# Performance work log

Measured on AMD Instinct MI355X. Metric: run time of the kernel, lower is better.

## Reference

```python
import jax, jax.numpy as jnp
import numpy as np

C_CT, C_MRI, C_OUT = 64, 64, 64
B, D, H, W = 1, 8, 32, 32


def setup_inputs() -> dict:
    key = jax.random.key(0)
    ks = jax.random.split(key, 18)
    s = 0.05
    inp = {
        "ct_features": jax.random.normal(ks[0], (B, C_CT, D, H, W), jnp.float32),
        "mri_features": jax.random.normal(ks[1], (B, C_MRI, D, H, W), jnp.float32),
        # 1x1x1 Conv3d == per-voxel linear: weight (out, in), bias (out,)
        "wq_ct": jax.random.normal(ks[2], (C_OUT, C_CT), jnp.float32) * s,
        "bq_ct": jax.random.normal(ks[3], (C_OUT,), jnp.float32) * s,
        "wk_mri": jax.random.normal(ks[4], (C_OUT, C_MRI), jnp.float32) * s,
        "bk_mri": jax.random.normal(ks[5], (C_OUT,), jnp.float32) * s,
        "wv_mri": jax.random.normal(ks[6], (C_OUT, C_MRI), jnp.float32) * s,
        "bv_mri": jax.random.normal(ks[7], (C_OUT,), jnp.float32) * s,
        "wq_mri": jax.random.normal(ks[8], (C_OUT, C_MRI), jnp.float32) * s,
        "bq_mri": jax.random.normal(ks[9], (C_OUT,), jnp.float32) * s,
        "wk_ct": jax.random.normal(ks[10], (C_OUT, C_CT), jnp.float32) * s,
        "bk_ct": jax.random.normal(ks[11], (C_OUT,), jnp.float32) * s,
        "wv_ct": jax.random.normal(ks[12], (C_OUT, C_CT), jnp.float32) * s,
        "bv_ct": jax.random.normal(ks[13], (C_OUT,), jnp.float32) * s,
        "wo": jax.random.normal(ks[14], (C_OUT, 2 * C_OUT), jnp.float32) * s,
        "bo": jax.random.normal(ks[15], (C_OUT,), jnp.float32) * s,
    }
    return inp


def _proj(x_flat, w, b):
    # x_flat: (B, Cin, N); 1x1x1 conv -> (B, Cout, N)
    return jnp.einsum("oc,bcn->bon", w, x_flat) + b[None, :, None]


def _forward(ct, mri, wq_ct, bq_ct, wk_mri, bk_mri, wv_mri, bv_mri,
             wq_mri, bq_mri, wk_ct, bk_ct, wv_ct, bv_ct, wo, bo):
    b, _, d, h, w = ct.shape
    n = d * h * w
    ct_f = ct.reshape(b, ct.shape[1], n)
    mri_f = mri.reshape(b, mri.shape[1], n)
    scale = 1.0 / np.sqrt(C_OUT).astype(np.float32)

    # CT queries attend over MRI keys/values
    ct_q = _proj(ct_f, wq_ct, bq_ct)      # (B, C, N)
    mri_k = _proj(mri_f, wk_mri, bk_mri)  # (B, C, N)
    mri_v = _proj(mri_f, wv_mri, bv_mri)  # (B, C, N)
    attn_ct = jax.nn.softmax(jnp.einsum("bci,bcj->bij", ct_q, mri_k) * scale, axis=-1)
    ct_att = jnp.einsum("bcj,bij->bci", mri_v, attn_ct)  # (B, C, N)

    # MRI queries attend over CT keys/values
    mri_q = _proj(mri_f, wq_mri, bq_mri)
    ct_k = _proj(ct_f, wk_ct, bk_ct)
    ct_v = _proj(ct_f, wv_ct, bv_ct)
    attn_mri = jax.nn.softmax(jnp.einsum("bci,bcj->bij", mri_q, ct_k) * scale, axis=-1)
    mri_att = jnp.einsum("bcj,bij->bci", ct_v, attn_mri)

    fused = jnp.concatenate([ct_att, mri_att], axis=1)  # (B, 2C, N)
    out = _proj(fused, wo, bo)  # (B, C, N)
    return out.reshape(b, C_OUT, d, h, w)


def reference(ct_features, mri_features, wq_ct, bq_ct, wk_mri, bk_mri,
              wv_mri, bv_mri, wq_mri, bq_mri, wk_ct, bk_ct, wv_ct, bv_ct,
              wo, bo):
    return _forward(ct_features, mri_features, wq_ct, bq_ct, wk_mri, bk_mri,
                    wv_mri, bv_mri, wq_mri, bq_mri, wk_ct, bk_ct,
                    wv_ct, bv_ct, wo, bo)
```

## Files before the change

kernel.cpp:

```cpp
#include <hip/hip_runtime.h>
#include <stdint.h>

constexpr int N = 8192;
constexpr float QSCALE = 0.18033688011112042f;
constexpr int SPLIT = 4;

typedef __attribute__((ext_vector_type(4))) float f32x4;
typedef __attribute__((ext_vector_type(16))) float f32x16;
typedef __attribute__((ext_vector_type(4))) unsigned int u32x4;
typedef __attribute__((ext_vector_type(2))) unsigned int u32x2;
typedef __attribute__((ext_vector_type(4))) unsigned short u16x4;
typedef __attribute__((ext_vector_type(8))) __bf16 bf16x8;

__device__ inline unsigned short f2bf(float f) {
  unsigned u = __builtin_bit_cast(unsigned, f);
  u += 0x7FFFu + ((u >> 16) & 1u);
  return (unsigned short)(u >> 16);
}
__device__ inline float bf2f(unsigned short u) {
  return __builtin_bit_cast(float, (unsigned)u << 16);
}
__device__ inline unsigned cvtpk(float a, float b) {
  unsigned r;
  asm("v_cvt_pk_bf16_f32 %0, %1, %2" : "=v"(r) : "v"(a), "v"(b));
  return r;
}

__device__ inline void mfma32(f32x16& d, u32x4 a, u32x4 b) {
  d = __builtin_amdgcn_mfma_f32_32x32x16_bf16(
      __builtin_bit_cast(bf16x8, a), __builtin_bit_cast(bf16x8, b), d, 0, 0, 0);
}
__device__ inline void gload16(const void* src, void* lds) {
  __builtin_amdgcn_global_load_lds(
      (const __attribute__((address_space(1))) unsigned int*)src,
      (__attribute__((address_space(3))) unsigned int*)lds, 16, 0, 0);
}

struct ProjArgs {
  const float* x[6];
  const float* w[6];
  const float* b[6];
  unsigned short* o[6];
  int mode[6];
  float scale[6];
};

__global__ __launch_bounds__(256) void proj_kernel(ProjArgs A) {
  const int p = blockIdx.y;
  const float* __restrict__ x = A.x[p];
  const float* __restrict__ w = A.w[p];
  const float* __restrict__ bias = A.b[p];
  unsigned short* __restrict__ out = A.o[p];
  const int n0 = blockIdx.x * 64;
  __shared__ float Xs[64][64];
  __shared__ float Ws[64][64];
  const int t = threadIdx.x;
#pragma unroll
  for (int i = 0; i < 4; i++) {
    int s = t + i * 256;
    ((u32x4*)Ws)[s] = ((const u32x4*)w)[s];
  }
#pragma unroll
  for (int i = 0; i < 4; i++) {
    int s = t + i * 256;
    int c = s >> 4, nc = s & 15;
    *(u32x4*)&Xs[c][nc * 4] = *(const u32x4*)&x[c * N + n0 + nc * 4];
  }
  __syncthreads();
  const int n = t & 63, h = t >> 6;
  float acc[16];
#pragma unroll
  for (int o = 0; o < 16; o++) acc[o] = bias[h * 16 + o];
  for (int c = 0; c < 64; c++) {
    float xv = Xs[c][n];
#pragma unroll
    for (int o = 0; o < 16; o++) acc[o] = fmaf(Ws[h * 16 + o][c], xv, acc[o]);
  }
  const float sc = A.scale[p];
  if (A.mode[p] == 0) {
    unsigned short* po = out + (size_t)(n0 + n) * 64 + h * 16;
#pragma unroll
    for (int o = 0; o < 16; o++) po[o] = f2bf(acc[o] * sc);
  } else {
#pragma unroll
    for (int o = 0; o < 16; o++) out[(size_t)(h * 16 + o) * N + n0 + n] = f2bf(acc[o] * sc);
  }
}

__global__ __launch_bounds__(256, 2) void attn_kernel(
    const unsigned short* __restrict__ Q0, const unsigned short* __restrict__ K0,
    const unsigned short* __restrict__ V0, const unsigned short* __restrict__ Q1,
    const unsigned short* __restrict__ K1, const unsigned short* __restrict__ V1,
    unsigned short* __restrict__ Opart, float* __restrict__ Lsum) {
  const int bid = blockIdx.x;
  const int slice = bid & 7;
  const int qb = bid >> 3;
  const int dir = slice >> 2;
  const int chunk = slice & 3;
  const unsigned short* __restrict__ Q = dir ? Q1 : Q0;
  const unsigned short* __restrict__ K = dir ? K1 : K0;
  const unsigned short* __restrict__ V = dir ? V1 : V0;

  __shared__ char smem[33280];

  const int t = threadIdx.x;
  const int lane = t & 63, w = t >> 6;
  const int qsub = w >> 1, jsub = w & 1;
  const int hi = lane >> 5, l31 = lane & 31;
  const int kvbase = chunk * 2048;

  const int srowoff = lane >> 3;
  const int swzb = ((lane & 7) ^ (lane >> 3)) * 16;
  const char* const Kc = (const char*)K;
  const char* const Vc = (const char*)V;

#define STAGE(jtile, slot)                                                     \
  do {                                                                         \
    const int j0s = kvbase + (jtile) * 64;                                     \
    _Pragma("unroll") for (int i = 0; i < 2; i++) {                            \
      const int row = (w * 2 + i) * 8 + srowoff;                               \
      gload16(Kc + (size_t)(j0s + row) * 128 + swzb,                           \
              smem + (slot) * 8192 + (w * 2 + i) * 1024);                      \
      gload16(Vc + (size_t)row * (N * 2) + (size_t)j0s * 2 + swzb,             \
              smem + 16384 + (slot) * 8192 + (w * 2 + i) * 1024);              \
    }                                                                          \
  } while (0)

  u32x4 qf[2][4];
#pragma unroll
  for (int qs = 0; qs < 2; qs++) {
    const int qrow = qb * 128 + qsub * 64 + qs * 32 + l31;
#pragma unroll
    for (int ks = 0; ks < 4; ks++)
      qf[qs][ks] = *(const u32x4*)((const char*)Q + (size_t)qrow * 128 + (2 * ks + hi) * 16);
  }

  f32x16 acc[2][2];
#pragma unroll
  for (int cb = 0; cb < 2; cb++)
#pragma unroll
    for (int qs = 0; qs < 2; qs++)
#pragma unroll
      for (int r = 0; r < 16; r++) acc[cb][qs][r] = 0.f;
  float lpart[2] = {0.f, 0.f};

  STAGE(0, 0);
  for (int jt = 0; jt < 32; ++jt) {
    asm volatile("s_waitcnt vmcnt(0)" ::: "memory");
    __builtin_amdgcn_s_barrier();
    __builtin_amdgcn_sched_barrier(0);
    const int cur = jt & 1;
    if (jt + 1 < 32) STAGE(jt + 1, cur ^ 1);
    char* const Kl = smem + cur * 8192;
    char* const Vl = smem + 16384 + cur * 8192;

    u32x4 kf[4];
    {
      const int row = jsub * 32 + l31;
      const int rs = (row & 7) << 4;
#pragma unroll
      for (int ks = 0; ks < 4; ks++)
        kf[ks] = *(const u32x4*)(Kl + row * 128 + (((2 * ks + hi) * 16) ^ rs));
    }

    f32x16 st[2];
#pragma unroll
    for (int qs = 0; qs < 2; qs++)
#pragma unroll
      for (int r = 0; r < 16; r++) st[qs][r] = 0.f;
    __builtin_amdgcn_s_setprio(1);
#pragma unroll
    for (int ks = 0; ks < 4; ks++) {
      mfma32(st[0], kf[ks], qf[0][ks]);
      mfma32(st[1], kf[ks], qf[1][ks]);
    }
    __builtin_amdgcn_s_setprio(0);

    u32x4 vf[2][2];
#pragma unroll
    for (int cb = 0; cb < 2; cb++) {
      const int row = cb * 32 + l31;
      const int rs = (row & 7) << 4;
#pragma unroll
      for (int js = 0; js < 2; js++)
        vf[cb][js] = *(const u32x4*)(Vl + row * 128 + (((jsub * 4 + js * 2 + hi) * 16) ^ rs));
    }

#pragma unroll
    for (int qs = 0; qs < 2; qs++) {
      float p[16];
#pragma unroll
      for (int r = 0; r < 16; r++) p[r] = __builtin_amdgcn_exp2f(st[qs][r]);
      lpart[qs] += (((p[0] + p[1]) + (p[2] + p[3])) + ((p[4] + p[5]) + (p[6] + p[7]))) +
                   (((p[8] + p[9]) + (p[10] + p[11])) + ((p[12] + p[13]) + (p[14] + p[15])));
      unsigned w00 = cvtpk(p[0], p[1]),   w01 = cvtpk(p[2], p[3]);
      unsigned w10 = cvtpk(p[4], p[5]),   w11 = cvtpk(p[6], p[7]);
      unsigned w20 = cvtpk(p[8], p[9]),   w21 = cvtpk(p[10], p[11]);
      unsigned w30 = cvtpk(p[12], p[13]), w31 = cvtpk(p[14], p[15]);
      asm volatile("v_permlane32_swap_b32 %0, %1" : "+v"(w00), "+v"(w10));
      asm volatile("v_permlane32_swap_b32 %0, %1" : "+v"(w01), "+v"(w11));
      asm volatile("v_permlane32_swap_b32 %0, %1" : "+v"(w20), "+v"(w30));
      asm volatile("v_permlane32_swap_b32 %0, %1" : "+v"(w21), "+v"(w31));
      u32x4 pf0, pf1;
      pf0[0] = w00; pf0[1] = w01; pf0[2] = w10; pf0[3] = w11;
      pf1[0] = w20; pf1[1] = w21; pf1[2] = w30; pf1[3] = w31;
      __builtin_amdgcn_s_setprio(1);
      mfma32(acc[0][qs], vf[0][0], pf0);
      mfma32(acc[1][qs], vf[1][0], pf0);
      mfma32(acc[0][qs], vf[0][1], pf1);
      mfma32(acc[1][qs], vf[1][1], pf1);
      __builtin_amdgcn_s_setprio(0);
    }
  }
#undef STAGE

#pragma unroll
  for (int qs = 0; qs < 2; qs++) lpart[qs] += __shfl_xor(lpart[qs], 32);

  __syncthreads();
  char* const obuf = smem + qsub * 16384;
  float* const mlb = (float*)(smem + 32768);
  if (jsub == 1) {
#pragma unroll
    for (int qs = 0; qs < 2; qs++) {
      const int qloc = qs * 32 + l31;
      const int qsw = (qloc & 7) << 4;
#pragma unroll
      for (int cb = 0; cb < 2; cb++)
#pragma unroll
        for (int a = 0; a < 4; a++) {
          const int ch0 = cb * 32 + 8 * a + 4 * hi;
          f32x4 v;
          v[0] = acc[cb][qs][4 * a];     v[1] = acc[cb][qs][4 * a + 1];
          v[2] = acc[cb][qs][4 * a + 2]; v[3] = acc[cb][qs][4 * a + 3];
          *(f32x4*)(obuf + qloc * 256 + ((ch0 * 4) ^ qsw)) = v;
        }
      if (hi == 0) mlb[qsub * 64 + qloc] = lpart[qs];
    }
  }
  __syncthreads();
  if (jsub == 0) {
#pragma unroll
    for (int qs = 0; qs < 2; qs++) {
      const int qloc = qs * 32 + l31;
      const int qsw = (qloc & 7) << 4;
      const int qg = qb * 128 + qsub * 64 + qloc;
      const size_t pbase = ((size_t)slice * N + qg) * 64;
#pragma unroll
      for (int cb = 0; cb < 2; cb++)
#pragma unroll
        for (int a = 0; a < 4; a++) {
          const int ch0 = cb * 32 + 8 * a + 4 * hi;
          f32x4 oo = *(const f32x4*)(obuf + qloc * 256 + ((ch0 * 4) ^ qsw));
          u32x2 pk;
          pk[0] = cvtpk(acc[cb][qs][4 * a] + oo[0], acc[cb][qs][4 * a + 1] + oo[1]);
          pk[1] = cvtpk(acc[cb][qs][4 * a + 2] + oo[2], acc[cb][qs][4 * a + 3] + oo[3]);
          *(u32x2*)(Opart + pbase + ch0) = pk;
        }
      if (hi == 0) Lsum[(size_t)slice * N + qg] = lpart[qs] + mlb[qsub * 64 + qloc];
    }
  }
}

__global__ __launch_bounds__(256) void oproj_kernel(
    const unsigned short* __restrict__ Opart, const float* __restrict__ Lsum,
    const float* __restrict__ wo, const float* __restrict__ bo,
    float* __restrict__ out) {
  __shared__ float Fs[128][32];
  __shared__ float Ws[64][128];
  const int t = threadIdx.x;
  const int n0 = blockIdx.x * 32;
#pragma unroll
  for (int i = 0; i < 8; i++) {
    int s = t + i * 256;
    ((u32x4*)Ws)[s] = ((const u32x4*)wo)[s];
  }
  const int q = t & 31;
  const int cg = t >> 5;
#pragma unroll
  for (int dir = 0; dir < 2; dir++) {
    float lt = 0.f;
#pragma unroll
    for (int c = 0; c < 4; c++) lt += Lsum[(size_t)(dir * SPLIT + c) * N + n0 + q];
    const float rD = 1.0f / lt;
#pragma unroll
    for (int i = 0; i < 2; i++) {
      const int ch4 = cg * 2 + i;
      float s0 = 0.f, s1 = 0.f, s2 = 0.f, s3 = 0.f;
#pragma unroll
      for (int c = 0; c < 4; c++) {
        u16x4 v = *(const u16x4*)(Opart +
            ((size_t)(dir * SPLIT + c) * N + n0 + q) * 64 + ch4 * 4);
        s0 += bf2f(v[0]); s1 += bf2f(v[1]); s2 += bf2f(v[2]); s3 += bf2f(v[3]);
      }
      Fs[dir * 64 + ch4 * 4 + 0][q] = s0 * rD;
      Fs[dir * 64 + ch4 * 4 + 1][q] = s1 * rD;
      Fs[dir * 64 + ch4 * 4 + 2][q] = s2 * rD;
      Fs[dir * 64 + ch4 * 4 + 3][q] = s3 * rD;
    }
  }
  __syncthreads();
  const int n = t & 31, h = t >> 5;
  float acc[8];
#pragma unroll
  for (int o = 0; o < 8; o++) acc[o] = bo[h * 8 + o];
  for (int ch = 0; ch < 128; ch++) {
    float fv = Fs[ch][n];
#pragma unroll
    for (int o = 0; o < 8; o++) acc[o] = fmaf(Ws[h * 8 + o][ch], fv, acc[o]);
  }
#pragma unroll
  for (int o = 0; o < 8; o++) out[(size_t)(h * 8 + o) * N + n0 + n] = acc[o];
}

extern "C" void kernel_launch(void* const* d_in, const int* in_sizes, int n_in,
                              void* d_out, int out_size, void* d_ws, size_t ws_size,
                              hipStream_t stream) {
  const float* ct     = (const float*)d_in[0];
  const float* mri    = (const float*)d_in[1];
  const float* wq_ct  = (const float*)d_in[2];
  const float* bq_ct  = (const float*)d_in[3];
  const float* wk_mri = (const float*)d_in[4];
  const float* bk_mri = (const float*)d_in[5];
  const float* wv_mri = (const float*)d_in[6];
  const float* bv_mri = (const float*)d_in[7];
  const float* wq_mri = (const float*)d_in[8];
  const float* bq_mri = (const float*)d_in[9];
  const float* wk_ct  = (const float*)d_in[10];
  const float* bk_ct  = (const float*)d_in[11];
  const float* wv_ct  = (const float*)d_in[12];
  const float* bv_ct  = (const float*)d_in[13];
  const float* wo     = (const float*)d_in[14];
  const float* bo     = (const float*)d_in[15];

  char* ws = (char*)d_ws;
  const size_t MB = (size_t)1 << 20;
  unsigned short* Qt_ct  = (unsigned short*)(ws + 0 * MB);
  unsigned short* Kt_mri = (unsigned short*)(ws + 1 * MB);
  unsigned short* V_mri  = (unsigned short*)(ws + 2 * MB);
  unsigned short* Qt_mri = (unsigned short*)(ws + 3 * MB);
  unsigned short* Kt_ct  = (unsigned short*)(ws + 4 * MB);
  unsigned short* V_ct   = (unsigned short*)(ws + 5 * MB);
  unsigned short* Opart  = (unsigned short*)(ws + 6 * MB);
  float* Lsum            = (float*)(ws + 14 * MB);

  ProjArgs A;
  A.x[0] = ct;  A.w[0] = wq_ct;  A.b[0] = bq_ct;  A.o[0] = Qt_ct;  A.mode[0] = 0; A.scale[0] = QSCALE;
  A.x[1] = mri; A.w[1] = wk_mri; A.b[1] = bk_mri; A.o[1] = Kt_mri; A.mode[1] = 0; A.scale[1] = 1.f;
  A.x[2] = mri; A.w[2] = wv_mri; A.b[2] = bv_mri; A.o[2] = V_mri;  A.mode[2] = 1; A.scale[2] = 1.f;
  A.x[3] = mri; A.w[3] = wq_mri; A.b[3] = bq_mri; A.o[3] = Qt_mri; A.mode[3] = 0; A.scale[3] = QSCALE;
  A.x[4] = ct;  A.w[4] = wk_ct;  A.b[4] = bk_ct;  A.o[4] = Kt_ct;  A.mode[4] = 0; A.scale[4] = 1.f;
  A.x[5] = ct;  A.w[5] = wv_ct;  A.b[5] = bv_ct;  A.o[5] = V_ct;   A.mode[5] = 1; A.scale[5] = 1.f;

  proj_kernel<<<dim3(128, 6), 256, 0, stream>>>(A);
  attn_kernel<<<dim3(512), 256, 0, stream>>>(Qt_ct, Kt_mri, V_mri,
                                             Qt_mri, Kt_ct, V_ct, Opart, Lsum);
  oproj_kernel<<<dim3(256), 256, 0, stream>>>(Opart, Lsum, wo, bo, (float*)d_out);
}
```

Before: 68.73 us.

## Load K/V fragments directly from global memory into registers instead of LDS staging

Removes the double-buffered LDS staging of K and V tiles, along with its per-iteration waitcnt and barrier. Each wave now loads its K fragments (prefetched one tile ahead) and V fragments straight from global memory into registers. This eliminates block-wide synchronization and LDS traffic. In exchange, global loads become less coalesced: the V loads use row strides of N*2 bytes, the two waves sharing a jsub read the same K/V redundantly, and the V-load latency is exposed within each iteration.

```diff
diff --git a/kernel.cpp b/kernel.cpp
--- a/kernel.cpp
+++ b/kernel.cpp
@@ -29,11 +29,6 @@
 __device__ inline void mfma32(f32x16& d, u32x4 a, u32x4 b) {
   d = __builtin_amdgcn_mfma_f32_32x32x16_bf16(
       __builtin_bit_cast(bf16x8, a), __builtin_bit_cast(bf16x8, b), d, 0, 0, 0);
-}
-__device__ inline void gload16(const void* src, void* lds) {
-  __builtin_amdgcn_global_load_lds(
-      (const __attribute__((address_space(1))) unsigned int*)src,
-      (__attribute__((address_space(3))) unsigned int*)lds, 16, 0, 0);
 }
 
 struct ProjArgs {
@@ -108,21 +103,23 @@
   const int qsub = w >> 1, jsub = w & 1;
   const int hi = lane >> 5, l31 = lane & 31;
   const int kvbase = chunk * 2048;
-
-  const int srowoff = lane >> 3;
-  const int swzb = ((lane & 7) ^ (lane >> 3)) * 16;
   const char* const Kc = (const char*)K;
   const char* const Vc = (const char*)V;
 
-#define STAGE(jtile, slot)                                                     \
+#define LOADK(jt, kf)                                                          \
   do {                                                                         \
-    const int j0s = kvbase + (jtile) * 64;                                     \
-    _Pragma("unroll") for (int i = 0; i < 2; i++) {                            \
-      const int row = (w * 2 + i) * 8 + srowoff;                               \
-      gload16(Kc + (size_t)(j0s + row) * 128 + swzb,                           \
-              smem + (slot) * 8192 + (w * 2 + i) * 1024);                      \
-      gload16(Vc + (size_t)row * (N * 2) + (size_t)j0s * 2 + swzb,             \
-              smem + 16384 + (slot) * 8192 + (w * 2 + i) * 1024);              \
+    const size_t row_ = (size_t)(kvbase + (jt) * 64 + jsub * 32 + l31);        \
+    _Pragma("unroll") for (int ks = 0; ks < 4; ks++)                           \
+      kf[ks] = *(const u32x4*)(Kc + row_ * 128 + (2 * ks + hi) * 16);          \
+  } while (0)
+#define LOADV(jt, vf)                                                          \
+  do {                                                                         \
+    const int jb_ = kvbase + (jt) * 64 + jsub * 32;                            \
+    _Pragma("unroll") for (int cb = 0; cb < 2; cb++) {                         \
+      const size_t vr_ = (size_t)(cb * 32 + l31) * (N * 2);                    \
+      _Pragma("unroll") for (int js = 0; js < 2; js++)                         \
+        vf[cb][js] = *(const u32x4*)(Vc + vr_ +                                \
+                                     (size_t)(jb_ + (js * 2 + hi) * 8) * 2);   \
     }                                                                          \
   } while (0)
 
@@ -144,75 +141,55 @@
       for (int r = 0; r < 16; r++) acc[cb][qs][r] = 0.f;
   float lpart[2] = {0.f, 0.f};
 
-  STAGE(0, 0);
-  for (int jt = 0; jt < 32; ++jt) {
-    asm volatile("s_waitcnt vmcnt(0)" ::: "memory");
-    __builtin_amdgcn_s_barrier();
-    __builtin_amdgcn_sched_barrier(0);
-    const int cur = jt & 1;
-    if (jt + 1 < 32) STAGE(jt + 1, cur ^ 1);
-    char* const Kl = smem + cur * 8192;
-    char* const Vl = smem + 16384 + cur * 8192;
-
-    u32x4 kf[4];
-    {
-      const int row = jsub * 32 + l31;
-      const int rs = (row & 7) << 4;
-#pragma unroll
-      for (int ks = 0; ks < 4; ks++)
-        kf[ks] = *(const u32x4*)(Kl + row * 128 + (((2 * ks + hi) * 16) ^ rs));
-    }
-
-    f32x16 st[2];
-#pragma unroll
-    for (int qs = 0; qs < 2; qs++)
-#pragma unroll
-      for (int r = 0; r < 16; r++) st[qs][r] = 0.f;
-    __builtin_amdgcn_s_setprio(1);
-#pragma unroll
-    for (int ks = 0; ks < 4; ks++) {
-      mfma32(st[0], kf[ks], qf[0][ks]);
-      mfma32(st[1], kf[ks], qf[1][ks]);
-    }
-    __builtin_amdgcn_s_setprio(0);
-
-    u32x4 vf[2][2];
-#pragma unroll
-    for (int cb = 0; cb < 2; cb++) {
-      const int row = cb * 32 + l31;
-      const int rs = (row & 7) << 4;
-#pragma unroll
-      for (int js = 0; js < 2; js++)
-        vf[cb][js] = *(const u32x4*)(Vl + row * 128 + (((jsub * 4 + js * 2 + hi) * 16) ^ rs));
-    }
-
-#pragma unroll
-    for (int qs = 0; qs < 2; qs++) {
-      float p[16];
-#pragma unroll
-      for (int r = 0; r < 16; r++) p[r] = __builtin_amdgcn_exp2f(st[qs][r]);
-      lpart[qs] += (((p[0] + p[1]) + (p[2] + p[3])) + ((p[4] + p[5]) + (p[6] + p[7]))) +
-                   (((p[8] + p[9]) + (p[10] + p[11])) + ((p[12] + p[13]) + (p[14] + p[15])));
-      unsigned w00 = cvtpk(p[0], p[1]),   w01 = cvtpk(p[2], p[3]);
-      unsigned w10 = cvtpk(p[4], p[5]),   w11 = cvtpk(p[6], p[7]);
-      unsigned w20 = cvtpk(p[8], p[9]),   w21 = cvtpk(p[10], p[11]);
-      unsigned w30 = cvtpk(p[12], p[13]), w31 = cvtpk(p[14], p[15]);
-      asm volatile("v_permlane32_swap_b32 %0, %1" : "+v"(w00), "+v"(w10));
-      asm volatile("v_permlane32_swap_b32 %0, %1" : "+v"(w01), "+v"(w11));
-      asm volatile("v_permlane32_swap_b32 %0, %1" : "+v"(w20), "+v"(w30));
-      asm volatile("v_permlane32_swap_b32 %0, %1" : "+v"(w21), "+v"(w31));
-      u32x4 pf0, pf1;
-      pf0[0] = w00; pf0[1] = w01; pf0[2] = w10; pf0[3] = w11;
-      pf1[0] = w20; pf1[1] = w21; pf1[2] = w30; pf1[3] = w31;
-      __builtin_amdgcn_s_setprio(1);
-      mfma32(acc[0][qs], vf[0][0], pf0);
-      mfma32(acc[1][qs], vf[1][0], pf0);
-      mfma32(acc[0][qs], vf[0][1], pf1);
-      mfma32(acc[1][qs], vf[1][1], pf1);
-      __builtin_amdgcn_s_setprio(0);
-    }
-  }
-#undef STAGE
+#define BODY(jt, kfC, kfN)                                                     \
+  do {                                                                         \
+    u32x4 vf[2][2];                                                            \
+    LOADV(jt, vf);                                     \
+    if ((jt) + 1 < 32) LOADK((jt) + 1, kfN);           \
+    f32x16 st[2];                                                              \
+    _Pragma("unroll") for (int qs = 0; qs < 2; qs++)                           \
+      _Pragma("unroll") for (int r = 0; r < 16; r++) st[qs][r] = 0.f;          \
+    __builtin_amdgcn_s_setprio(1);                                             \
+    _Pragma("unroll") for (int ks = 0; ks < 4; ks++) {                         \
+      mfma32(st[0], kfC[ks], qf[0][ks]);                                       \
+      mfma32(st[1], kfC[ks], qf[1][ks]);                                       \
+    }                                                                          \
+    __builtin_amdgcn_s_setprio(0);                                             \
+    _Pragma("unroll") for (int qs = 0; qs < 2; qs++) {                         \
+      float p[16];                                                             \
+      _Pragma("unroll") for (int r = 0; r < 16; r++)                           \
+        p[r] = __builtin_amdgcn_exp2f(st[qs][r]);                              \
+      lpart[qs] += (((p[0]+p[1])+(p[2]+p[3]))+((p[4]+p[5])+(p[6]+p[7]))) +     \
+                   (((p[8]+p[9])+(p[10]+p[11]))+((p[12]+p[13])+(p[14]+p[15])));\
+      unsigned w00 = cvtpk(p[0], p[1]),   w01 = cvtpk(p[2], p[3]);             \
+      unsigned w10 = cvtpk(p[4], p[5]),   w11 = cvtpk(p[6], p[7]);             \
+      unsigned w20 = cvtpk(p[8], p[9]),   w21 = cvtpk(p[10], p[11]);           \
+      unsigned w30 = cvtpk(p[12], p[13]), w31 = cvtpk(p[14], p[15]);           \
+      asm volatile("v_permlane32_swap_b32 %0, %1" : "+v"(w00), "+v"(w10));     \
+      asm volatile("v_permlane32_swap_b32 %0, %1" : "+v"(w01), "+v"(w11));     \
+      asm volatile("v_permlane32_swap_b32 %0, %1" : "+v"(w20), "+v"(w30));     \
+      asm volatile("v_permlane32_swap_b32 %0, %1" : "+v"(w21), "+v"(w31));     \
+      u32x4 pf0, pf1;                                                          \
+      pf0[0] = w00; pf0[1] = w01; pf0[2] = w10; pf0[3] = w11;                  \
+      pf1[0] = w20; pf1[1] = w21; pf1[2] = w30; pf1[3] = w31;                  \
+      __builtin_amdgcn_s_setprio(1);                                           \
+      mfma32(acc[0][qs], vf[0][0], pf0);                                       \
+      mfma32(acc[1][qs], vf[1][0], pf0);                                       \
+      mfma32(acc[0][qs], vf[0][1], pf1);                                       \
+      mfma32(acc[1][qs], vf[1][1], pf1);                                       \
+      __builtin_amdgcn_s_setprio(0);                                           \
+    }                                                                          \
+  } while (0)
+
+  u32x4 kfA[4], kfB[4];
+  LOADK(0, kfA);
+  for (int jt = 0; jt < 32; jt += 2) {
+    BODY(jt, kfA, kfB);
+    BODY(jt + 1, kfB, kfA);
+  }
+#undef BODY
+#undef LOADK
+#undef LOADV
 
 #pragma unroll
   for (int qs = 0; qs < 2; qs++) lpart[qs] += __shfl_xor(lpart[qs], 32);
```

After: 91.80 us. 33.6% more time.
